# Performance work log

Measured on AMD Instinct MI355X. Metric: run time of the kernel, lower is better.

Reference implementation:

```python
import jax, jax.numpy as jnp
import numpy as np
import math

B, S, H, NH = 8, 1024, 1024, 16
DH = H // NH


def _ln(x, g, b, eps=1e-5):
    m = x.mean(-1, keepdims=True)
    v = ((x - m) ** 2).mean(-1, keepdims=True)
    return (x - m) / jnp.sqrt(v + eps) * g + b


def _attn(qx, kx, vx, wq, bq, wk, bk, wv, bv, wo, bo, mask):
    b = qx.shape[0]
    def heads(t, w, bias):
        return (t @ w + bias).reshape(b, -1, NH, DH).transpose(0, 2, 1, 3)
    q, k, v = heads(qx, wq, bq), heads(kx, wk, bk), heads(vx, wv, bv)
    corr = jnp.einsum('bhqd,bhkd->bhqk', q, k) / math.sqrt(DH)  # [B,NH,Sq,Sk]
    corr = jnp.where(mask[:, None, :, None] == 0, -1e9, corr)  # mask per query row
    p = jax.nn.softmax(corr, axis=-1)
    o = jnp.einsum('bhqk,bhkd->bhqd', p, v).transpose(0, 2, 1, 3).reshape(b, -1, H)
    return o @ wo + bo


def setup_inputs() -> dict:
    key = jax.random.key(0)
    ks = jax.random.split(key, 16)
    d = {}
    d['x'] = jax.random.normal(ks[0], (B, S, H), jnp.float32)
    d['h'] = jax.random.normal(ks[1], (B, S, H), jnp.float32)
    d['mask'] = jnp.ones((B, S), jnp.int32)
    wnames = ['sa_wq', 'sa_wk', 'sa_wv', 'sa_wo', 'ca_wq', 'ca_wk', 'ca_wv', 'ca_wo', 'ff_w1', 'ff_w2']
    for i, n in enumerate(wnames):
        d[n] = jax.random.normal(ks[2 + i], (H, H), jnp.float32) * 0.02
    for n in ['sa_bq', 'sa_bk', 'sa_bv', 'sa_bo', 'ca_bq', 'ca_bk', 'ca_bv', 'ca_bo', 'ff_b1', 'ff_b2']:
        d[n] = jnp.zeros((H,), jnp.float32)
    for n in ['ln1', 'ln2', 'ln3', 'lnh', 'ff_ln']:
        d[n + '_g'] = jnp.ones((H,), jnp.float32)
        d[n + '_b'] = jnp.zeros((H,), jnp.float32)
    return d


def reference(x, h, mask, ln1_g, ln1_b, ln2_g, ln2_b, ln3_g, ln3_b, lnh_g, lnh_b,
              sa_wq, sa_bq, sa_wk, sa_bk, sa_wv, sa_bv, sa_wo, sa_bo,
              ca_wq, ca_bq, ca_wk, ca_bk, ca_wv, ca_bv, ca_wo, ca_bo,
              ff_w1, ff_b1, ff_w2, ff_b2, ff_ln_g, ff_ln_b):
    # self-attention block (pre-LN, residual)
    xn = _ln(x, ln1_g, ln1_b)
    hidden_in = _attn(xn, xn, xn, sa_wq, sa_bq, sa_wk, sa_bk, sa_wv, sa_bv, sa_wo, sa_bo, mask) + x
    # cross-attention block
    mid_n = _ln(hidden_in, ln2_g, ln2_b)
    hn = _ln(h, lnh_g, lnh_b)
    hidden_mid = _attn(mid_n, hn, hn, ca_wq, ca_bq, ca_wk, ca_bk, ca_wv, ca_bv, ca_wo, ca_bo, mask) + hidden_in
    # position-wise FFN (Conv1d k=1 == pointwise linear) with its own LN+residual
    y = _ln(hidden_mid, ln3_g, ln3_b)
    ff = jax.nn.relu(y @ ff_w1 + ff_b1) @ ff_w2 + ff_b2
    ffo = _ln(ff + y, ff_ln_g, ff_ln_b)
    return ffo + hidden_mid
```

## Files before the change

### kernel.cpp

```cpp
#include <hip/hip_runtime.h>

typedef unsigned short u16;
typedef unsigned int u32;
typedef float f32x4 __attribute__((ext_vector_type(4)));
typedef float f32x16 __attribute__((ext_vector_type(16)));
typedef __bf16 bf16x8 __attribute__((ext_vector_type(8)));

#define MFMA16(a, b, c) __builtin_amdgcn_mfma_f32_16x16x32_bf16(a, b, c, 0, 0, 0)
#define MFMA32(a, b, c) __builtin_amdgcn_mfma_f32_32x32x16_bf16(a, b, c, 0, 0, 0)
#define PLSWAP(x, y) asm volatile("v_permlane32_swap_b32 %0, %1" : "+v"(x), "+v"(y))
#define CFENCE() asm volatile("" ::: "memory")
#define BAR()                         \
    {                                 \
        CFENCE();                     \
        __builtin_amdgcn_s_barrier(); \
        CFENCE();                     \
    }
#define WAITV(n) asm volatile("s_waitcnt vmcnt(" #n ")" ::: "memory")

__device__ __forceinline__ u16 f2b(float f) {
    u32 u = __builtin_bit_cast(u32, f);
    u += 0x7fffu + ((u >> 16) & 1u);
    return (u16)(u >> 16);
}

__device__ __forceinline__ u32 pk2(float a, float b) {
    union { u32 u; __bf16 h[2]; } r;
    r.h[0] = (__bf16)a; r.h[1] = (__bf16)b;
    return r.u;
}

__device__ __forceinline__ void gload16(const u16* g, u16* l) {
    __builtin_amdgcn_global_load_lds((const __attribute__((address_space(1))) void*)g,
                                     (__attribute__((address_space(3))) void*)l, 16, 0, 0);
}

struct W10 { const float* p[10]; };
__global__ __launch_bounds__(256) void tcvt_k(W10 wp, u16* __restrict__ WT0) {
    const float* __restrict__ Wm = wp.p[blockIdx.z];
    u16* __restrict__ WT = WT0 + (size_t)blockIdx.z * 1048576;
    __shared__ float t[32][33];
    int bx = blockIdx.x, by = blockIdx.y;
    int tx = threadIdx.x, ty = threadIdx.y;
#pragma unroll
    for (int j = 0; j < 32; j += 8)
        t[ty + j][tx] = Wm[(size_t)(by * 32 + ty + j) * 1024 + bx * 32 + tx];
    __syncthreads();
#pragma unroll
    for (int j = 0; j < 32; j += 8)
        WT[(size_t)(bx * 32 + ty + j) * 1024 + by * 32 + tx] = f2b(t[tx][ty + j]);
}

__global__ __launch_bounds__(256) void vtr_k(const u16* __restrict__ Vg, int ldv, u16* __restrict__ VT) {
    __shared__ u16 t[32][34];
    int bx = blockIdx.x, by = blockIdx.y, b = blockIdx.z;
    int tx = threadIdx.x, ty = threadIdx.y;
#pragma unroll
    for (int j = 0; j < 32; j += 8)
        t[ty + j][tx] = Vg[(size_t)(b * 1024 + by * 32 + ty + j) * ldv + bx * 32 + tx];
    __syncthreads();
#pragma unroll
    for (int j = 0; j < 32; j += 8)
        VT[(size_t)(b * 1024 + bx * 32 + ty + j) * 1024 + by * 32 + tx] = t[tx][ty + j];
}

template <int MODE>
__global__ __launch_bounds__(256) void ln_k(const float* __restrict__ in1, const float* __restrict__ in2,
                                            const float* __restrict__ gg, const float* __restrict__ bb,
                                            const float* __restrict__ post,
                                            float* __restrict__ of, u16* __restrict__ ob) {
    int tid = threadIdx.x, lane = tid & 63, w = tid >> 6;
    int row = blockIdx.x * 4 + w;
    size_t base = (size_t)row * 1024 + lane * 16;
    float x[16];
#pragma unroll
    for (int i = 0; i < 4; i++) *(float4*)&x[i * 4] = *(const float4*)(in1 + base + i * 4);
    if constexpr (MODE & 1) {
#pragma unroll
        for (int i = 0; i < 4; i++) {
            float4 v = *(const float4*)(in2 + base + i * 4);
            x[i * 4] += v.x; x[i * 4 + 1] += v.y; x[i * 4 + 2] += v.z; x[i * 4 + 3] += v.w;
        }
    }
    float s1 = 0.f, s2 = 0.f;
#pragma unroll
    for (int i = 0; i < 16; i++) { s1 += x[i]; s2 += x[i] * x[i]; }
#pragma unroll
    for (int m = 1; m <= 32; m <<= 1) { s1 += __shfl_xor(s1, m); s2 += __shfl_xor(s2, m); }
    float mean = s1 * (1.0f / 1024.0f);
    float var = s2 * (1.0f / 1024.0f) - mean * mean;
    float rstd = rsqrtf(var + 1e-5f);
    float y[16];
#pragma unroll
    for (int i = 0; i < 4; i++) {
        float4 gv = *(const float4*)(gg + lane * 16 + i * 4);
        float4 bv = *(const float4*)(bb + lane * 16 + i * 4);
        y[i * 4 + 0] = (x[i * 4 + 0] - mean) * rstd * gv.x + bv.x;
        y[i * 4 + 1] = (x[i * 4 + 1] - mean) * rstd * gv.y + bv.y;
        y[i * 4 + 2] = (x[i * 4 + 2] - mean) * rstd * gv.z + bv.z;
        y[i * 4 + 3] = (x[i * 4 + 3] - mean) * rstd * gv.w + bv.w;
    }
    if constexpr (MODE & 2) {
#pragma unroll
        for (int i = 0; i < 4; i++) {
            float4 o;
            o.x = y[i * 4]; o.y = y[i * 4 + 1]; o.z = y[i * 4 + 2]; o.w = y[i * 4 + 3];
            if constexpr (MODE & 8) {
                float4 p = *(const float4*)(post + base + i * 4);
                o.x += p.x; o.y += p.y; o.z += p.z; o.w += p.w;
            }
            *(float4*)(of + base + i * 4) = o;
        }
    }
    if constexpr (MODE & 4) {
#pragma unroll
        for (int i = 0; i < 2; i++) {
            uint4 pk;
            pk.x = pk2(y[i * 8 + 0], y[i * 8 + 1]);
            pk.y = pk2(y[i * 8 + 2], y[i * 8 + 3]);
            pk.z = pk2(y[i * 8 + 4], y[i * 8 + 5]);
            pk.w = pk2(y[i * 8 + 6], y[i * 8 + 7]);
            *(uint4*)(ob + base + i * 8) = pk;
        }
    }
}

template <int EPI, int WN, int NBN>
__global__ __launch_bounds__(512) void gemm512_k(const u16* __restrict__ A, int lda,
                                                 const u16* __restrict__ WT,
                                                 const float* __restrict__ b0, const float* __restrict__ b1,
                                                 const float* __restrict__ b2,
                                                 float sc0, float sc1, float sc2,
                                                 const float* __restrict__ res,
                                                 void* __restrict__ outp, int ldc) {
    constexpr int ASZ = 8192;
    constexpr int BSZ = (WN == 4) ? 8192 : 4096;
    constexpr int SLOT = ASZ + BSZ;
    constexpr int MR = (WN == 4) ? 8 : 4;
    constexpr int WRS = (WN == 4) ? 128 : 64;
    __shared__ u16 lds[3 * SLOT];
    u16* ldsb = &lds[0];

    int id = blockIdx.x;
    constexpr int NWG = 32 * NBN;
    constexpr int CPX = NWG / 8;
    int swz = (id & 7) * CPX + (id >> 3);
    int bm = swz / NBN, bn = swz % NBN;
    const int m0 = bm * 256, n0 = bn * (WN * 64);
    int tid = threadIdx.x, lane = tid & 63, w = tid >> 6;
    int col = lane & 15, fg = lane >> 4;
    int wr = (WN == 4) ? (w >> 2) : (w >> 1);
    int wc = w & (WN - 1);

    int swzL = ((col * 32) + fg * 8) ^ ((col >> 1) << 3);
    int aoff0 = wr * WRS * 32 + swzL;
    int boff0 = ASZ + wc * 64 * 32 + swzL;

    int r = tid >> 2, g = tid & 3;
    int gr = r ^ ((r >> 3) & 1);
    int gc = g ^ ((r >> 1) & 3);
    const u16* pA = A + (size_t)(m0 + gr) * lda + gc * 8;
    const u16* pB = WT + (size_t)(n0 + gr) * 1024 + gc * 8;

#define STGA(t2, snO)                                                                 \
    {                                                                                 \
        gload16(pA + (size_t)(t2) * 32, ldsb + (snO) + w * 512);                      \
        gload16(pA + (size_t)(t2) * 32 + (size_t)128 * lda, ldsb + (snO) + 4096 + w * 512); \
    }
#define STGB(t2, snO)                                                                 \
    {                                                                                 \
        gload16(pB + (size_t)(t2) * 32, ldsb + (snO) + ASZ + w * 512);                \
        if constexpr (WN == 4) {                                                      \
            gload16(pB + (size_t)(t2) * 32 + (size_t)128 * 1024, ldsb + (snO) + ASZ + 4096 + w * 512); \
        }                                                                             \
    }

    f32x4 acc[MR][4];
#pragma unroll
    for (int m = 0; m < MR; m++)
#pragma unroll
        for (int n = 0; n < 4; n++) acc[m][n] = (f32x4){0.f, 0.f, 0.f, 0.f};

    STGA(0, 0); STGB(0, 0);
    STGA(1, SLOT); STGB(1, SLOT);
    if constexpr (WN == 4) { WAITV(4); } else { WAITV(3); }
    BAR();

    int sc = 0, sn = 2;
    for (int t = 0; t < 32; ++t) {
        int sCur = sc * SLOT, sNxt = sn * SLOT;
        bf16x8 a0[4], bfv[WN];
#pragma unroll
        for (int m = 0; m < 4; m++) a0[m] = *(const bf16x8*)&ldsb[sCur + aoff0 + m * 512];
#pragma unroll
        for (int n = 0; n < WN; n++) bfv[n] = *(const bf16x8*)&ldsb[sCur + boff0 + n * 512];
        if (t < 30) STGA(t + 2, sNxt);
        BAR();
        __builtin_amdgcn_s_setprio(1);
#pragma unroll
        for (int m = 0; m < 4; m++)
#pragma unroll
            for (int n = 0; n < WN; n++) acc[m][n] = MFMA16(a0[m], bfv[n], acc[m][n]);
        __builtin_amdgcn_s_setprio(0);
        BAR();
        if constexpr (WN == 4) {
            bf16x8 a1[4];
#pragma unroll
            for (int m = 0; m < 4; m++) a1[m] = *(const bf16x8*)&ldsb[sCur + aoff0 + (m + 4) * 512];
            if (t < 30) STGB(t + 2, sNxt);
            BAR();
            __builtin_amdgcn_s_setprio(1);
#pragma unroll
            for (int m = 0; m < 4; m++)
#pragma unroll
                for (int n = 0; n < 4; n++) acc[m + 4][n] = MFMA16(a1[m], bfv[n], acc[m + 4][n]);
            __builtin_amdgcn_s_setprio(0);
            if (t < 30) { WAITV(4); } else if (t == 30) { WAITV(0); }
            BAR();
        } else {
            bf16x8 b2[2];
#pragma unroll
            for (int n = 0; n < 2; n++) b2[n] = *(const bf16x8*)&ldsb[sCur + boff0 + (n + 2) * 512];
            if (t < 30) STGB(t + 2, sNxt);
            BAR();
            __builtin_amdgcn_s_setprio(1);
#pragma unroll
            for (int m = 0; m < 4; m++)
#pragma unroll
                for (int n = 0; n < 2; n++) acc[m][n + 2] = MFMA16(a0[m], b2[n], acc[m][n + 2]);
            __builtin_amdgcn_s_setprio(0);
            if (t < 30) { WAITV(3); } else if (t == 30) { WAITV(0); }
            BAR();
        }
        sc = (sc == 2) ? 0 : sc + 1;
        sn = (sn == 2) ? 0 : sn + 1;
    }
#undef STGA
#undef STGB

    int seg = n0 >> 10;
    const float* bp = (seg == 0) ? b0 : (seg == 1 ? b1 : b2);
    float sg = (seg == 0) ? sc0 : (seg == 1 ? sc1 : sc2);
    int nseg = n0 & 1023;
    float bv[4];
#pragma unroll
    for (int n = 0; n < 4; n++) bv[n] = bp[nseg + wc * 64 + n * 16 + col];
#pragma unroll
    for (int m = 0; m < MR; m++) {
#pragma unroll
        for (int rr = 0; rr < 4; rr++) {
            int row = m0 + wr * WRS + m * 16 + fg * 4 + rr;
#pragma unroll
            for (int n = 0; n < 4; n++) {
                int c = n0 + wc * 64 + n * 16 + col;
                size_t idx = (size_t)row * ldc + c;
                float v = (acc[m][n][rr] + bv[n]) * sg;
                if constexpr (EPI == 0) ((u16*)outp)[idx] = f2b(v);
                else if constexpr (EPI == 1) ((u16*)outp)[idx] = f2b(fmaxf(v, 0.f));
                else if constexpr (EPI == 2) ((float*)outp)[idx] = v + res[idx];
            }
        }
    }
}

template <int EPI, int NBN>
__global__ __launch_bounds__(256) void gemm256_k(const u16* __restrict__ A, int lda,
                                                 const u16* __restrict__ WT,
                                                 const float* __restrict__ b0,
                                                 float sc0,
                                                 const float* __restrict__ res,
                                                 void* __restrict__ outp, int ldc) {
    constexpr int SLOT = 8192;
    __shared__ u16 lds[3 * SLOT];
    int id = blockIdx.x;
    constexpr int NWG = 64 * NBN;
    constexpr int CPX = NWG / 8;
    int swz = (id & 7) * CPX + (id >> 3);
    int bm = swz / NBN, bn = swz % NBN;
    const int m0 = bm * 128, n0 = bn * 128;
    int tid = threadIdx.x, lane = tid & 63, w = tid >> 6;
    int col = lane & 15, fg = lane >> 4;
    int wr = w >> 1, wc = w & 1;

    int swzL = ((col * 32) + fg * 8) ^ ((col >> 1) << 3);
    int aoff0 = wr * 64 * 32 + swzL;
    int boff0 = 4096 + wc * 64 * 32 + swzL;

    int r = tid >> 2, g = tid & 3;
    int gr = r ^ ((r >> 3) & 1);
    int gc = g ^ ((r >> 1) & 3);
    const u16* pA = A + (size_t)(m0 + gr) * lda + gc * 8;
    const u16* pB = WT + (size_t)(n0 + gr) * 1024 + gc * 8;

#define STGA(t2, snO)                                                                     \
    {                                                                                     \
        gload16(pA + (size_t)(t2) * 32, lds + (snO) + w * 512);                           \
        gload16(pA + (size_t)(t2) * 32 + (size_t)64 * lda, lds + (snO) + 2048 + w * 512); \
    }
#define STGB(t2, snO)                                                                             \
    {                                                                                             \
        gload16(pB + (size_t)(t2) * 32, lds + (snO) + 4096 + w * 512);                            \
        gload16(pB + (size_t)(t2) * 32 + (size_t)64 * 1024, lds + (snO) + 4096 + 2048 + w * 512); \
    }

    f32x4 acc[4][4];
#pragma unroll
    for (int m = 0; m < 4; m++)
#pragma unroll
        for (int n = 0; n < 4; n++) acc[m][n] = (f32x4){0.f, 0.f, 0.f, 0.f};

    STGA(0, 0); STGB(0, 0);
    STGA(1, SLOT); STGB(1, SLOT);
    WAITV(4);
    BAR();

    int sc = 0, sn = 2;
    for (int t = 0; t < 32; ++t) {
        int sCur = sc * SLOT, sNxt = sn * SLOT;
        bf16x8 a0[4], bfv[2];
#pragma unroll
        for (int m = 0; m < 4; m++) a0[m] = *(const bf16x8*)&lds[sCur + aoff0 + m * 512];
#pragma unroll
        for (int n = 0; n < 2; n++) bfv[n] = *(const bf16x8*)&lds[sCur + boff0 + n * 512];
        if (t < 30) STGA(t + 2, sNxt);
        BAR();
        __builtin_amdgcn_s_setprio(1);
#pragma unroll
        for (int m = 0; m < 4; m++)
#pragma unroll
            for (int n = 0; n < 2; n++) acc[m][n] = MFMA16(a0[m], bfv[n], acc[m][n]);
        __builtin_amdgcn_s_setprio(0);
        BAR();
        bf16x8 b2[2];
#pragma unroll
        for (int n = 0; n < 2; n++) b2[n] = *(const bf16x8*)&lds[sCur + boff0 + (n + 2) * 512];
        if (t < 30) STGB(t + 2, sNxt);
        BAR();
        __builtin_amdgcn_s_setprio(1);
#pragma unroll
        for (int m = 0; m < 4; m++)
#pragma unroll
            for (int n = 0; n < 2; n++) acc[m][n + 2] = MFMA16(a0[m], b2[n], acc[m][n + 2]);
        __builtin_amdgcn_s_setprio(0);
        if (t < 30) { WAITV(4); } else if (t == 30) { WAITV(0); }
        BAR();
        sc = (sc == 2) ? 0 : sc + 1;
        sn = (sn == 2) ? 0 : sn + 1;
    }
#undef STGA
#undef STGB

    float bv[4];
#pragma unroll
    for (int n = 0; n < 4; n++) bv[n] = b0[(n0 & 1023) + wc * 64 + n * 16 + col];
#pragma unroll
    for (int m = 0; m < 4; m++) {
#pragma unroll
        for (int rr = 0; rr < 4; rr++) {
            int row = m0 + wr * 64 + m * 16 + fg * 4 + rr;
#pragma unroll
            for (int n = 0; n < 4; n++) {
                int c = n0 + wc * 64 + n * 16 + col;
                size_t idx = (size_t)row * ldc + c;
                float v = (acc[m][n][rr] + bv[n]) * sc0;
                if constexpr (EPI == 0) ((u16*)outp)[idx] = f2b(v);
                else if constexpr (EPI == 1) ((u16*)outp)[idx] = f2b(fmaxf(v, 0.f));
                else if constexpr (EPI == 2) ((float*)outp)[idx] = v + res[idx];
            }
        }
    }
}

__global__ __launch_bounds__(512) void attn_k(const u16* __restrict__ Q, int ldq,
                                              const u16* __restrict__ Kc, int ldk,
                                              const u16* __restrict__ VT,
                                              const int* __restrict__ mask,
                                              u16* __restrict__ O, int ldo) {
    const int S = 1024;
    int gid = blockIdx.x;
    int bq = gid >> 7, hh = (gid >> 3) & 15, bb = gid & 7;
    int tid = threadIdx.x, lane = tid & 63, w = tid >> 6;
    int q = lane & 31, hl = lane >> 5;
    int q0w = bq * 256 + w * 32;

    __shared__ u16 sm[18432];
#define KT(b, r, c) sm[(b) * 9216 + (r) * 72 + (c)]
#define VTL(b, r, c) sm[(b) * 9216 + 4608 + (r) * 72 + (c)]

    const u16* Qrow = Q + ((size_t)bb * S + q0w + q) * ldq + hh * 64;
    bool mneg = (mask[bb * S + q0w + q] == 0);
    bf16x8 qf[4];
#pragma unroll
    for (int c = 0; c < 4; c++) {
        qf[c] = *(const bf16x8*)(Qrow + c * 16 + hl * 8);
        if (mneg) qf[c] = (bf16x8)(__bf16)0.f;
    }

    float l = 0.f;
    f32x16 oa[2];
#pragma unroll
    for (int i = 0; i < 16; i++) { oa[0][i] = 0.f; oa[1][i] = 0.f; }

    int kk = tid >> 3, ks = tid & 7;
    const u16* gK = Kc + ((size_t)bb * S + kk) * ldk + hh * 64 + ks * 8;
    const u16* gVT = VT + ((size_t)(bb * 16 + hh) * 64 + kk) * 1024 + ks * 8;
    uint4 kr0, vr0;

#define LOADT(t)                                              \
    {                                                         \
        kr0 = *(const uint4*)(gK + (size_t)(t) * 64 * ldk);   \
        vr0 = *(const uint4*)(gVT + (size_t)(t) * 64);        \
    }
#define STORET(bf)                            \
    {                                         \
        *(uint4*)&KT(bf, kk, ks * 8) = kr0;   \
        *(uint4*)&VTL(bf, kk, ks * 8) = vr0;  \
    }

    LOADT(0);
    STORET(0);

    for (int t = 0; t < 16; ++t) {
        int cur = t & 1;
        if (t < 15) LOADT(t + 1);
        __syncthreads();

        f32x16 sc[2];
#pragma unroll
        for (int i = 0; i < 16; i++) { sc[0][i] = 0.f; sc[1][i] = 0.f; }
        __builtin_amdgcn_s_setprio(1);
#pragma unroll
        for (int st = 0; st < 2; st++)
#pragma unroll
            for (int c = 0; c < 4; c++) {
                bf16x8 kf = *(const bf16x8*)&KT(cur, st * 32 + q, c * 16 + hl * 8);
                sc[st] = MFMA32(kf, qf[c], sc[st]);
            }
        __builtin_amdgcn_s_setprio(0);

#pragma unroll
        for (int st = 0; st < 2; st++)
#pragma unroll
            for (int rr = 0; rr < 16; rr++) sc[st][rr] = exp2f(sc[st][rr]);
        float ts[8];
#pragma unroll
        for (int i = 0; i < 8; i++)
            ts[i] = (sc[0][i] + sc[0][i + 8]) + (sc[1][i] + sc[1][i + 8]);
#pragma unroll
        for (int i = 0; i < 4; i++) ts[i] += ts[i + 4];
        l += (ts[0] + ts[2]) + (ts[1] + ts[3]);

        __builtin_amdgcn_s_setprio(1);
#pragma unroll
        for (int st = 0; st < 2; st++) {
            u32 wv[8];
#pragma unroll
            for (int j = 0; j < 8; j++) wv[j] = pk2(sc[st][2 * j], sc[st][2 * j + 1]);
            PLSWAP(wv[0], wv[2]); PLSWAP(wv[1], wv[3]);
            PLSWAP(wv[4], wv[6]); PLSWAP(wv[5], wv[7]);
#pragma unroll
            for (int c = 0; c < 2; c++) {
                union { u32 u[4]; bf16x8 v; } pb;
                pb.u[0] = wv[c * 4 + 0]; pb.u[1] = wv[c * 4 + 1];
                pb.u[2] = wv[c * 4 + 2]; pb.u[3] = wv[c * 4 + 3];
#pragma unroll
                for (int dd = 0; dd < 2; dd++) {
                    bf16x8 vf = *(const bf16x8*)&VTL(cur, dd * 32 + q, st * 32 + c * 16 + hl * 8);
                    oa[dd] = MFMA32(vf, pb.v, oa[dd]);
                }
            }
        }
        __builtin_amdgcn_s_setprio(0);

        if (t < 15) STORET(cur ^ 1);
    }

    l += __shfl_xor(l, 32);
    __syncthreads();
    float inv = 1.0f / l;
    u16* otw = sm + w * 2304;
#pragma unroll
    for (int dd = 0; dd < 2; dd++)
#pragma unroll
        for (int rr = 0; rr < 16; rr++) {
            int d = (rr & 3) + 8 * (rr >> 2) + 4 * hl + 32 * dd;
            otw[q * 72 + d] = f2b(oa[dd][rr] * inv);
        }
    __syncthreads();
    size_t obase = ((size_t)bb * S + q0w) * ldo + hh * 64;
#pragma unroll
    for (int i = 0; i < 4; i++) {
        int row = i * 8 + (lane >> 3);
        uint4 vdat = *(const uint4*)&otw[row * 72 + (lane & 7) * 8];
        *(uint4*)(O + obase + (size_t)row * ldo + (lane & 7) * 8) = vdat;
    }
#undef KT
#undef VTL
#undef LOADT
#undef STORET
}

extern "C" void kernel_launch(void* const* d_in, const int* in_sizes, int n_in,
                              void* d_out, int out_size, void* d_ws, size_t ws_size,
                              hipStream_t stream) {
    (void)in_sizes; (void)n_in; (void)out_size; (void)ws_size;
    const float* x = (const float*)d_in[0];
    const float* h = (const float*)d_in[1];
    const int* mask = (const int*)d_in[2];
    const float* W[10];
    const float* Bv[10];
    for (int i = 0; i < 10; i++) { W[i] = (const float*)d_in[3 + i]; Bv[i] = (const float*)d_in[13 + i]; }
    const float *ln1g = (const float*)d_in[23], *ln1b = (const float*)d_in[24];
    const float *ln2g = (const float*)d_in[25], *ln2b = (const float*)d_in[26];
    const float *ln3g = (const float*)d_in[27], *ln3b = (const float*)d_in[28];
    const float *lnhg = (const float*)d_in[29], *lnhb = (const float*)d_in[30];
    const float *flng = (const float*)d_in[31], *flnb = (const float*)d_in[32];

    const float SCLE = 0.18033688011112042f;

    char* ws = (char*)d_ws;
    size_t off = 0;
    auto alloc = [&](size_t bytes) -> char* {
        char* p = ws + off;
        off += (bytes + 255) & ~(size_t)255;
        return p;
    };
    const size_t MT = (size_t)8192 * 1024;
    u16* wtb = (u16*)alloc((size_t)10 * 1048576 * 2);
    u16* wt[10];
    for (int i = 0; i < 10; i++) wt[i] = wtb + (size_t)i * 1048576;
    u16* qkv = (u16*)alloc((size_t)8192 * 3072 * 2);
    u16* kv = qkv;
    u16* kb = qkv + (size_t)8192 * 2048;
    u16* bufA = (u16*)alloc(MT * 2);
    u16* qb   = (u16*)alloc(MT * 2);
    float* hid_in  = (float*)alloc(MT * 4);
    float* hid_mid = (float*)alloc(MT * 4);
    float* yf      = (float*)alloc(MT * 4);
    u16* hn = (u16*)yf;
    u16* vt_sa = bufA;
    u16* vt_ca = (u16*)hid_mid;
    float* outF = (float*)d_out;

    W10 wp;
    for (int i = 0; i < 10; i++) wp.p[i] = W[i];
    tcvt_k<<<dim3(32, 32, 10), dim3(32, 8), 0, stream>>>(wp, wtb);

    ln_k<4><<<2048, 256, 0, stream>>>(x, nullptr, ln1g, ln1b, nullptr, nullptr, bufA);
    gemm512_k<0, 2, 24><<<768, 512, 0, stream>>>(bufA, 1024, wt[0], Bv[0], Bv[1], Bv[2], SCLE, 1.f, 1.f, nullptr, qkv, 3072);
    vtr_k<<<dim3(32, 32, 8), dim3(32, 8), 0, stream>>>(qkv + 2048, 3072, vt_sa);
    attn_k<<<512, 512, 0, stream>>>(qkv, 3072, qkv + 1024, 3072, vt_sa, mask, qkv, 3072);
    gemm256_k<2, 8><<<512, 256, 0, stream>>>(qkv, 3072, wt[3], Bv[3], 1.f, x, hid_in, 1024);

    ln_k<4><<<2048, 256, 0, stream>>>(hid_in, nullptr, ln2g, ln2b, nullptr, nullptr, bufA);
    ln_k<4><<<2048, 256, 0, stream>>>(h, nullptr, lnhg, lnhb, nullptr, nullptr, hn);
    gemm256_k<0, 8><<<512, 256, 0, stream>>>(bufA, 1024, wt[4], Bv[4], SCLE, nullptr, qb, 1024);
    gemm512_k<0, 2, 16><<<512, 512, 0, stream>>>(hn, 1024, wt[5], Bv[5], Bv[6], Bv[6], 1.f, 1.f, 1.f, nullptr, kv, 2048);
    vtr_k<<<dim3(32, 32, 8), dim3(32, 8), 0, stream>>>(kv + 1024, 2048, vt_ca);
    attn_k<<<512, 512, 0, stream>>>(qb, 1024, kv, 2048, vt_ca, mask, qb, 1024);
    gemm256_k<2, 8><<<512, 256, 0, stream>>>(qb, 1024, wt[7], Bv[7], 1.f, hid_in, hid_mid, 1024);

    ln_k<6><<<2048, 256, 0, stream>>>(hid_mid, nullptr, ln3g, ln3b, nullptr, yf, bufA);
    gemm256_k<1, 8><<<512, 256, 0, stream>>>(bufA, 1024, wt[8], Bv[8], 1.f, nullptr, kb, 1024);
    gemm256_k<2, 8><<<512, 256, 0, stream>>>(kb, 1024, wt[9], Bv[9], 1.f, yf, hid_in, 1024);
    ln_k<10><<<2048, 256, 0, stream>>>(hid_in, nullptr, flng, flnb, hid_mid, outF, nullptr);
}
```

Before: 457.3 us.

## Widen attention KV tiles to 128 keys and remap layernorm to one row per block

```diff
diff --git a/kernel.cpp b/kernel.cpp
--- a/kernel.cpp
+++ b/kernel.cpp
@@ -69,59 +69,46 @@
                                             const float* __restrict__ gg, const float* __restrict__ bb,
                                             const float* __restrict__ post,
                                             float* __restrict__ of, u16* __restrict__ ob) {
-    int tid = threadIdx.x, lane = tid & 63, w = tid >> 6;
-    int row = blockIdx.x * 4 + w;
-    size_t base = (size_t)row * 1024 + lane * 16;
-    float x[16];
-#pragma unroll
-    for (int i = 0; i < 4; i++) *(float4*)&x[i * 4] = *(const float4*)(in1 + base + i * 4);
+    int row = blockIdx.x, tid = threadIdx.x;
+    size_t base = (size_t)row * 1024 + tid * 4;
+    float4 x = *(const float4*)(in1 + base);
     if constexpr (MODE & 1) {
-#pragma unroll
-        for (int i = 0; i < 4; i++) {
-            float4 v = *(const float4*)(in2 + base + i * 4);
-            x[i * 4] += v.x; x[i * 4 + 1] += v.y; x[i * 4 + 2] += v.z; x[i * 4 + 3] += v.w;
-        }
-    }
-    float s1 = 0.f, s2 = 0.f;
-#pragma unroll
-    for (int i = 0; i < 16; i++) { s1 += x[i]; s2 += x[i] * x[i]; }
-#pragma unroll
-    for (int m = 1; m <= 32; m <<= 1) { s1 += __shfl_xor(s1, m); s2 += __shfl_xor(s2, m); }
+        float4 x2 = *(const float4*)(in2 + base);
+        x.x += x2.x; x.y += x2.y; x.z += x2.z; x.w += x2.w;
+    }
+    float s1 = x.x + x.y + x.z + x.w;
+    float s2 = x.x * x.x + x.y * x.y + x.z * x.z + x.w * x.w;
+#pragma unroll
+    for (int m = 32; m >= 1; m >>= 1) { s1 += __shfl_xor(s1, m); s2 += __shfl_xor(s2, m); }
+    __shared__ float r1[4], r2[4];
+    int lane = tid & 63, w = tid >> 6;
+    if (lane == 0) { r1[w] = s1; r2[w] = s2; }
+    __syncthreads();
+    s1 = r1[0] + r1[1] + r1[2] + r1[3];
+    s2 = r2[0] + r2[1] + r2[2] + r2[3];
     float mean = s1 * (1.0f / 1024.0f);
     float var = s2 * (1.0f / 1024.0f) - mean * mean;
     float rstd = rsqrtf(var + 1e-5f);
-    float y[16];
-#pragma unroll
-    for (int i = 0; i < 4; i++) {
-        float4 gv = *(const float4*)(gg + lane * 16 + i * 4);
-        float4 bv = *(const float4*)(bb + lane * 16 + i * 4);
-        y[i * 4 + 0] = (x[i * 4 + 0] - mean) * rstd * gv.x + bv.x;
-        y[i * 4 + 1] = (x[i * 4 + 1] - mean) * rstd * gv.y + bv.y;
-        y[i * 4 + 2] = (x[i * 4 + 2] - mean) * rstd * gv.z + bv.z;
-        y[i * 4 + 3] = (x[i * 4 + 3] - mean) * rstd * gv.w + bv.w;
-    }
+    float4 gv = *(const float4*)(gg + tid * 4);
+    float4 bv = *(const float4*)(bb + tid * 4);
+    float y0 = (x.x - mean) * rstd * gv.x + bv.x;
+    float y1 = (x.y - mean) * rstd * gv.y + bv.y;
+    float y2 = (x.z - mean) * rstd * gv.z + bv.z;
+    float y3 = (x.w - mean) * rstd * gv.w + bv.w;
     if constexpr (MODE & 2) {
-#pragma unroll
-        for (int i = 0; i < 4; i++) {
-            float4 o;
-            o.x = y[i * 4]; o.y = y[i * 4 + 1]; o.z = y[i * 4 + 2]; o.w = y[i * 4 + 3];
-            if constexpr (MODE & 8) {
-                float4 p = *(const float4*)(post + base + i * 4);
-                o.x += p.x; o.y += p.y; o.z += p.z; o.w += p.w;
-            }
-            *(float4*)(of + base + i * 4) = o;
+        float o0 = y0, o1 = y1, o2 = y2, o3 = y3;
+        if constexpr (MODE & 8) {
+            float4 p = *(const float4*)(post + base);
+            o0 += p.x; o1 += p.y; o2 += p.z; o3 += p.w;
         }
+        float4 o; o.x = o0; o.y = o1; o.z = o2; o.w = o3;
+        *(float4*)(of + base) = o;
     }
     if constexpr (MODE & 4) {
-#pragma unroll
-        for (int i = 0; i < 2; i++) {
-            uint4 pk;
-            pk.x = pk2(y[i * 8 + 0], y[i * 8 + 1]);
-            pk.y = pk2(y[i * 8 + 2], y[i * 8 + 3]);
-            pk.z = pk2(y[i * 8 + 4], y[i * 8 + 5]);
-            pk.w = pk2(y[i * 8 + 6], y[i * 8 + 7]);
-            *(uint4*)(ob + base + i * 8) = pk;
-        }
+        uint2 pk;
+        pk.x = (u32)f2b(y0) | ((u32)f2b(y1) << 16);
+        pk.y = (u32)f2b(y2) | ((u32)f2b(y3) << 16);
+        *(uint2*)(ob + base) = pk;
     }
 }
 
@@ -383,9 +370,9 @@
     int q = lane & 31, hl = lane >> 5;
     int q0w = bq * 256 + w * 32;
 
-    __shared__ u16 sm[18432];
-#define KT(b, r, c) sm[(b) * 9216 + (r) * 72 + (c)]
-#define VTL(b, r, c) sm[(b) * 9216 + 4608 + (r) * 72 + (c)]
+    __shared__ u16 sm[35840];
+#define KT(b, r, c) sm[(b) * 17920 + (r) * 72 + (c)]
+#define VTL(b, r, c) sm[(b) * 17920 + 9216 + (r) * 136 + (c)]
 
     const u16* Qrow = Q + ((size_t)bb * S + q0w + q) * ldq + hh * 64;
     bool mneg = (mask[bb * S + q0w + q] == 0);
@@ -401,78 +388,87 @@
 #pragma unroll
     for (int i = 0; i < 16; i++) { oa[0][i] = 0.f; oa[1][i] = 0.f; }
 
-    int kk = tid >> 3, ks = tid & 7;
-    const u16* gK = Kc + ((size_t)bb * S + kk) * ldk + hh * 64 + ks * 8;
-    const u16* gVT = VT + ((size_t)(bb * 16 + hh) * 64 + kk) * 1024 + ks * 8;
-    uint4 kr0, vr0;
-
-#define LOADT(t)                                              \
-    {                                                         \
-        kr0 = *(const uint4*)(gK + (size_t)(t) * 64 * ldk);   \
-        vr0 = *(const uint4*)(gVT + (size_t)(t) * 64);        \
-    }
-#define STORET(bf)                            \
-    {                                         \
-        *(uint4*)&KT(bf, kk, ks * 8) = kr0;   \
-        *(uint4*)&VTL(bf, kk, ks * 8) = vr0;  \
+    int kk = tid >> 2, k4 = tid & 3;
+    int vk = tid >> 3, v8 = tid & 7;
+    const u16* gK = Kc + ((size_t)bb * S + kk) * ldk + hh * 64 + k4 * 16;
+    const u16* gVT = VT + ((size_t)(bb * 16 + hh) * 64 + vk) * 1024 + v8 * 16;
+    uint4 kr0, kr1, vr0, vr1;
+
+#define LOADT(t)                                                   \
+    {                                                              \
+        const u16* pk_ = gK + (size_t)(t) * 128 * ldk;             \
+        kr0 = *(const uint4*)pk_; kr1 = *(const uint4*)(pk_ + 8);  \
+        const u16* pv_ = gVT + (size_t)(t) * 128;                  \
+        vr0 = *(const uint4*)pv_; vr1 = *(const uint4*)(pv_ + 8);  \
+    }
+#define STORET(bf)                                       \
+    {                                                    \
+        *(uint4*)&KT(bf, kk, k4 * 16) = kr0;             \
+        *(uint4*)&KT(bf, kk, k4 * 16 + 8) = kr1;         \
+        *(uint4*)&VTL(bf, vk, v8 * 16) = vr0;            \
+        *(uint4*)&VTL(bf, vk, v8 * 16 + 8) = vr1;        \
     }
 
     LOADT(0);
     STORET(0);
 
-    for (int t = 0; t < 16; ++t) {
+    for (int t = 0; t < 8; ++t) {
         int cur = t & 1;
-        if (t < 15) LOADT(t + 1);
+        if (t < 7) LOADT(t + 1);
         __syncthreads();
 
-        f32x16 sc[2];
-#pragma unroll
-        for (int i = 0; i < 16; i++) { sc[0][i] = 0.f; sc[1][i] = 0.f; }
-        __builtin_amdgcn_s_setprio(1);
-#pragma unroll
-        for (int st = 0; st < 2; st++)
-#pragma unroll
-            for (int c = 0; c < 4; c++) {
-                bf16x8 kf = *(const bf16x8*)&KT(cur, st * 32 + q, c * 16 + hl * 8);
-                sc[st] = MFMA32(kf, qf[c], sc[st]);
-            }
-        __builtin_amdgcn_s_setprio(0);
-
-#pragma unroll
-        for (int st = 0; st < 2; st++)
-#pragma unroll
-            for (int rr = 0; rr < 16; rr++) sc[st][rr] = exp2f(sc[st][rr]);
-        float ts[8];
-#pragma unroll
-        for (int i = 0; i < 8; i++)
-            ts[i] = (sc[0][i] + sc[0][i + 8]) + (sc[1][i] + sc[1][i + 8]);
-#pragma unroll
-        for (int i = 0; i < 4; i++) ts[i] += ts[i + 4];
-        l += (ts[0] + ts[2]) + (ts[1] + ts[3]);
-
-        __builtin_amdgcn_s_setprio(1);
-#pragma unroll
-        for (int st = 0; st < 2; st++) {
-            u32 wv[8];
-#pragma unroll
-            for (int j = 0; j < 8; j++) wv[j] = pk2(sc[st][2 * j], sc[st][2 * j + 1]);
-            PLSWAP(wv[0], wv[2]); PLSWAP(wv[1], wv[3]);
-            PLSWAP(wv[4], wv[6]); PLSWAP(wv[5], wv[7]);
-#pragma unroll
-            for (int c = 0; c < 2; c++) {
-                union { u32 u[4]; bf16x8 v; } pb;
-                pb.u[0] = wv[c * 4 + 0]; pb.u[1] = wv[c * 4 + 1];
-                pb.u[2] = wv[c * 4 + 2]; pb.u[3] = wv[c * 4 + 3];
-#pragma unroll
-                for (int dd = 0; dd < 2; dd++) {
-                    bf16x8 vf = *(const bf16x8*)&VTL(cur, dd * 32 + q, st * 32 + c * 16 + hl * 8);
-                    oa[dd] = MFMA32(vf, pb.v, oa[dd]);
+#pragma unroll
+        for (int sub = 0; sub < 2; ++sub) {
+            f32x16 sc[2];
+#pragma unroll
+            for (int i = 0; i < 16; i++) { sc[0][i] = 0.f; sc[1][i] = 0.f; }
+            __builtin_amdgcn_s_setprio(1);
+#pragma unroll
+            for (int st = 0; st < 2; st++)
+#pragma unroll
+                for (int c = 0; c < 4; c++) {
+                    bf16x8 kf = *(const bf16x8*)&KT(cur, sub * 64 + st * 32 + q, c * 16 + hl * 8);
+                    sc[st] = MFMA32(kf, qf[c], sc[st]);
+                }
+            __builtin_amdgcn_s_setprio(0);
+
+#pragma unroll
+            for (int st = 0; st < 2; st++)
+#pragma unroll
+                for (int rr = 0; rr < 16; rr++) sc[st][rr] = exp2f(sc[st][rr]);
+            float ts[8];
+#pragma unroll
+            for (int i = 0; i < 8; i++)
+                ts[i] = (sc[0][i] + sc[0][i + 8]) + (sc[1][i] + sc[1][i + 8]);
+#pragma unroll
+            for (int i = 0; i < 4; i++) ts[i] += ts[i + 4];
+            l += (ts[0] + ts[2]) + (ts[1] + ts[3]);
+
+            __builtin_amdgcn_s_setprio(1);
+#pragma unroll
+            for (int st = 0; st < 2; st++) {
+                u32 wv[8];
+#pragma unroll
+                for (int j = 0; j < 8; j++) wv[j] = pk2(sc[st][2 * j], sc[st][2 * j + 1]);
+                PLSWAP(wv[0], wv[2]); PLSWAP(wv[1], wv[3]);
+                PLSWAP(wv[4], wv[6]); PLSWAP(wv[5], wv[7]);
+#pragma unroll
+                for (int c = 0; c < 2; c++) {
+                    union { u32 u[4]; bf16x8 v; } pb;
+                    pb.u[0] = wv[c * 4 + 0]; pb.u[1] = wv[c * 4 + 1];
+                    pb.u[2] = wv[c * 4 + 2]; pb.u[3] = wv[c * 4 + 3];
+#pragma unroll
+                    for (int dd = 0; dd < 2; dd++) {
+                        bf16x8 vf = *(const bf16x8*)&VTL(cur, dd * 32 + q,
+                                                         sub * 64 + st * 32 + c * 16 + hl * 8);
+                        oa[dd] = MFMA32(vf, pb.v, oa[dd]);
+                    }
                 }
             }
+            __builtin_amdgcn_s_setprio(0);
         }
-        __builtin_amdgcn_s_setprio(0);
-
-        if (t < 15) STORET(cur ^ 1);
+
+        if (t < 7) STORET(cur ^ 1);
     }
 
     l += __shfl_xor(l, 32);
@@ -546,22 +542,22 @@
     for (int i = 0; i < 10; i++) wp.p[i] = W[i];
     tcvt_k<<<dim3(32, 32, 10), dim3(32, 8), 0, stream>>>(wp, wtb);
 
-    ln_k<4><<<2048, 256, 0, stream>>>(x, nullptr, ln1g, ln1b, nullptr, nullptr, bufA);
+    ln_k<4><<<8192, 256, 0, stream>>>(x, nullptr, ln1g, ln1b, nullptr, nullptr, bufA);
     gemm512_k<0, 2, 24><<<768, 512, 0, stream>>>(bufA, 1024, wt[0], Bv[0], Bv[1], Bv[2], SCLE, 1.f, 1.f, nullptr, qkv, 3072);
     vtr_k<<<dim3(32, 32, 8), dim3(32, 8), 0, stream>>>(qkv + 2048, 3072, vt_sa);
     attn_k<<<512, 512, 0, stream>>>(qkv, 3072, qkv + 1024, 3072, vt_sa, mask, qkv, 3072);
     gemm256_k<2, 8><<<512, 256, 0, stream>>>(qkv, 3072, wt[3], Bv[3], 1.f, x, hid_in, 1024);
 
-    ln_k<4><<<2048, 256, 0, stream>>>(hid_in, nullptr, ln2g, ln2b, nullptr, nullptr, bufA);
-    ln_k<4><<<2048, 256, 0, stream>>>(h, nullptr, lnhg, lnhb, nullptr, nullptr, hn);
+    ln_k<4><<<8192, 256, 0, stream>>>(hid_in, nullptr, ln2g, ln2b, nullptr, nullptr, bufA);
+    ln_k<4><<<8192, 256, 0, stream>>>(h, nullptr, lnhg, lnhb, nullptr, nullptr, hn);
     gemm256_k<0, 8><<<512, 256, 0, stream>>>(bufA, 1024, wt[4], Bv[4], SCLE, nullptr, qb, 1024);
     gemm512_k<0, 2, 16><<<512, 512, 0, stream>>>(hn, 1024, wt[5], Bv[5], Bv[6], Bv[6], 1.f, 1.f, 1.f, nullptr, kv, 2048);
     vtr_k<<<dim3(32, 32, 8), dim3(32, 8), 0, stream>>>(kv + 1024, 2048, vt_ca);
     attn_k<<<512, 512, 0, stream>>>(qb, 1024, kv, 2048, vt_ca, mask, qb, 1024);
     gemm256_k<2, 8><<<512, 256, 0, stream>>>(qb, 1024, wt[7], Bv[7], 1.f, hid_in, hid_mid, 1024);
 
-    ln_k<6><<<2048, 256, 0, stream>>>(hid_mid, nullptr, ln3g, ln3b, nullptr, yf, bufA);
+    ln_k<6><<<8192, 256, 0, stream>>>(hid_mid, nullptr, ln3g, ln3b, nullptr, yf, bufA);
     gemm256_k<1, 8><<<512, 256, 0, stream>>>(bufA, 1024, wt[8], Bv[8], 1.f, nullptr, kb, 1024);
     gemm256_k<2, 8><<<512, 256, 0, stream>>>(kb, 1024, wt[9], Bv[9], 1.f, yf, hid_in, 1024);
-    ln_k<10><<<2048, 256, 0, stream>>>(hid_in, nullptr, flng, flnb, hid_mid, outF, nullptr);
-}
+    ln_k<10><<<8192, 256, 0, stream>>>(hid_in, nullptr, flng, flnb, hid_mid, outF, nullptr);
+}
```

New measurement: 463.9 us. No clear change (+1.5%).
